# Kernel tuning notes

Hardware: AMD Instinct MI355X
Metric: run time of the kernel (lower is better)

The kernel has to match this reference:

```python
import jax, jax.numpy as jnp
import numpy as np

B, L, D, H = 2, 2048, 1024, 16
DK = D // H  # head_dim = 64


def setup_inputs() -> dict:
    key = jax.random.key(0)
    ks = jax.random.split(key, 12)
    init = lambda k, shape, fan_in: jax.random.uniform(k, shape, jnp.float32, -1.0, 1.0) / np.sqrt(fan_in)
    inp = {
        "query": jax.random.normal(ks[0], (B, L, D), jnp.float32),
        "key": jax.random.normal(ks[1], (B, L, D), jnp.float32),
        "value": jax.random.normal(ks[2], (B, L, D), jnp.float32),
        # causal mask [B, 1, L, L], True = attend
        "mask": jnp.broadcast_to(jnp.tril(jnp.ones((L, L), bool))[None, None], (B, 1, L, L)),
        "wq": init(ks[3], (D, D), D), "bq": jnp.zeros((D,), jnp.float32),
        "wk": init(ks[4], (D, D), D), "bk": jnp.zeros((D,), jnp.float32),
        "wv": init(ks[5], (D, D), D), "bv": jnp.zeros((D,), jnp.float32),
        "wo": init(ks[6], (D, D), D), "bo": jnp.zeros((D,), jnp.float32),
    }
    return inp


def reference(query, key, value, mask, wq, bq, wk, bk, wv, bv, wo, bo):
    b, l, d = query.shape
    split = lambda x: x.reshape(b, l, H, DK).transpose(0, 2, 1, 3)  # B H L dk
    Q = split(query @ wq + bq)
    K = split(key @ wk + bk)
    V = split(value @ wv + bv)
    scores = jnp.einsum("bhqd,bhkd->bhqk", Q, K) / jnp.sqrt(jnp.float32(DK))
    probs = jax.nn.softmax(scores, axis=-1, where=mask)  # masked-out rows contribute 0
    attn = jnp.einsum("bhqk,bhkd->bhqd", probs, V)
    out = attn.transpose(0, 2, 1, 3).reshape(b, l, d)  # B L D
    return out @ wo + bo
```

## Files before the change

kernel.cpp:

```cpp
#include <hip/hip_runtime.h>
#include <hip/hip_bf16.h>

typedef __bf16 bf16x8 __attribute__((ext_vector_type(8)));
typedef __bf16 bf16x4 __attribute__((ext_vector_type(4)));
typedef float floatx4 __attribute__((ext_vector_type(4)));

constexpr int Bn  = 2;
constexpr int Ln  = 2048;
constexpr int Dn  = 1024;
constexpr int Hn  = 16;
constexpr int DKn = 64;
constexpr int Mn  = Bn * Ln;

__device__ __forceinline__ void gload_lds16(const void* g, void* l) {
  __builtin_amdgcn_global_load_lds(
      (const __attribute__((address_space(1))) void*)g,
      (__attribute__((address_space(3))) void*)l, 16, 0, 0);
}

__global__ __launch_bounds__(256) void prep(
    const float* __restrict__ q, const float* __restrict__ k,
    const float* __restrict__ v,
    const float* __restrict__ wq, const float* __restrict__ wk,
    const float* __restrict__ wv, const float* __restrict__ wo,
    __hip_bfloat16* __restrict__ Abf, __hip_bfloat16* __restrict__ wT)
{
  const int z = blockIdx.z;
  __shared__ __bf16 tile[32][33];
  if (z < 3) {
    const float* src = z == 0 ? q : z == 1 ? k : v;
    __hip_bfloat16* d = Abf + (size_t)z * Mn * Dn;
    const int i = blockIdx.x * 256 + threadIdx.x;
    const float4 a = ((const float4*)src)[i * 2];
    const float4 b = ((const float4*)src)[i * 2 + 1];
    bf16x8 o;
    o[0] = (__bf16)a.x; o[1] = (__bf16)a.y; o[2] = (__bf16)a.z; o[3] = (__bf16)a.w;
    o[4] = (__bf16)b.x; o[5] = (__bf16)b.y; o[6] = (__bf16)b.z; o[7] = (__bf16)b.w;
    ((bf16x8*)d)[i] = o;
  } else {
    if (blockIdx.x >= 1024) return;
    const float* src = z == 3 ? wq : z == 4 ? wk : z == 5 ? wv : wo;
    __hip_bfloat16* dst = wT + (size_t)(z - 3) * Dn * Dn;
    const int bx = blockIdx.x & 31, by = blockIdx.x >> 5;
    const int tx = threadIdx.x & 31, ty = threadIdx.x >> 5;
    const int x = bx * 32 + tx, y = by * 32 + ty;
    for (int i = 0; i < 32; i += 8)
      tile[ty + i][tx] = (__bf16)src[(size_t)(y + i) * Dn + x];
    __syncthreads();
    const int x2 = by * 32 + tx, y2 = bx * 32 + ty;
    for (int i = 0; i < 32; i += 8)
      ((__bf16*)dst)[(size_t)(y2 + i) * Dn + x2] = tile[tx][ty + i];
  }
}

__global__ __launch_bounds__(256) void gemm_qkv(
    const __hip_bfloat16* __restrict__ Abf,
    const __hip_bfloat16* __restrict__ wT,
    const float* __restrict__ bq, const float* __restrict__ bk,
    const float* __restrict__ bv,
    __hip_bfloat16* __restrict__ Qp, __hip_bfloat16* __restrict__ Kp,
    __hip_bfloat16* __restrict__ Vt)
{
  constexpr int BK = 32;
  __shared__ __bf16 As[128][BK];
  __shared__ __bf16 Ws[128][BK];
  const int z = blockIdx.z;
  const __hip_bfloat16* A  = Abf + (size_t)z * Mn * Dn;
  const __hip_bfloat16* WT = wT  + (size_t)z * Dn * Dn;
  const float* bias = z == 0 ? bq : z == 1 ? bk : bv;

  const int m0 = blockIdx.x * 128;
  const int n0 = blockIdx.y * 128;
  const int tid  = threadIdx.x;
  const int lane = tid & 63;
  const int wave = tid >> 6;
  const int quad = lane >> 4;
  const int l16  = lane & 15;
  const int wm = (wave >> 1) * 64;
  const int wn = (wave & 1) * 64;
  const int srow = tid >> 2;
  const int scol = (tid & 3) * 8;

  floatx4 acc[4][4];
  for (int i = 0; i < 4; i++)
    for (int j = 0; j < 4; j++)
      acc[i][j] = (floatx4){0.f, 0.f, 0.f, 0.f};

  for (int k0 = 0; k0 < Dn; k0 += BK) {
    for (int half = 0; half < 2; half++) {
      gload_lds16(&A [(size_t)(m0 + srow + half * 64) * Dn + k0 + scol],
                  &As[srow + half * 64][scol]);
      gload_lds16(&WT[(size_t)(n0 + srow + half * 64) * Dn + k0 + scol],
                  &Ws[srow + half * 64][scol]);
    }
    __syncthreads();
    bf16x8 af[4], wf[4];
    for (int i = 0; i < 4; i++) af[i] = *(const bf16x8*)&As[wm + i * 16 + l16][quad * 8];
    for (int j = 0; j < 4; j++) wf[j] = *(const bf16x8*)&Ws[wn + j * 16 + l16][quad * 8];
    if (z == 2) {
      for (int i = 0; i < 4; i++)
        for (int j = 0; j < 4; j++)
          acc[i][j] = __builtin_amdgcn_mfma_f32_16x16x32_bf16(af[i], wf[j], acc[i][j], 0, 0, 0);
    } else {
      for (int i = 0; i < 4; i++)
        for (int j = 0; j < 4; j++)
          acc[i][j] = __builtin_amdgcn_mfma_f32_16x16x32_bf16(wf[j], af[i], acc[i][j], 0, 0, 0);
    }
    __syncthreads();
  }

  if (z == 2) {
    for (int j = 0; j < 4; j++) {
      const int n = n0 + wn + j * 16 + l16;
      const float bvv = bias[n];
      const int h = n >> 6, dk = n & 63;
      for (int i = 0; i < 4; i++) {
        const int m = m0 + wm + i * 16 + quad * 4;
        const int b = m >> 11, li = m & (Ln - 1);
        bf16x4 pk;
        for (int r = 0; r < 4; r++) pk[r] = (__bf16)(acc[i][j][r] + bvv);
        *(bf16x4*)&Vt[(((size_t)(b * Hn + h)) * DKn + dk) * Ln + li] = pk;
      }
    }
  } else {
    __hip_bfloat16* out = z == 0 ? Qp : Kp;
    for (int j = 0; j < 4; j++) {
      const int nq = n0 + wn + j * 16 + quad * 4;
      const float4 b4 = *(const float4*)&bias[nq];
      const int h = nq >> 6, dk = nq & 63;
      for (int i = 0; i < 4; i++) {
        const int m = m0 + wm + i * 16 + l16;
        const int b = m >> 11, li = m & (Ln - 1);
        bf16x4 pk;
        pk[0] = (__bf16)(acc[i][j][0] + b4.x);
        pk[1] = (__bf16)(acc[i][j][1] + b4.y);
        pk[2] = (__bf16)(acc[i][j][2] + b4.z);
        pk[3] = (__bf16)(acc[i][j][3] + b4.w);
        *(bf16x4*)&out[(((size_t)(b * Hn + h)) * Ln + li) * DKn + dk] = pk;
      }
    }
  }
}

__global__ __launch_bounds__(256) void gemm_out(
    const __hip_bfloat16* __restrict__ A,
    const __hip_bfloat16* __restrict__ WT,
    const float* __restrict__ bias,
    float* __restrict__ out)
{
  constexpr int BK = 32;
  __shared__ __bf16 As[128][BK];
  __shared__ __bf16 Ws[64][BK];
  const int m0 = blockIdx.x * 128;
  const int n0 = blockIdx.y * 64;
  const int tid  = threadIdx.x;
  const int lane = tid & 63;
  const int wave = tid >> 6;
  const int quad = lane >> 4;
  const int l16  = lane & 15;
  const int wm = (wave >> 1) * 64;
  const int wn = (wave & 1) * 32;
  const int srow = tid >> 2;
  const int scol = (tid & 3) * 8;

  floatx4 acc[4][2];
  for (int i = 0; i < 4; i++)
    for (int j = 0; j < 2; j++)
      acc[i][j] = (floatx4){0.f, 0.f, 0.f, 0.f};

  for (int k0 = 0; k0 < Dn; k0 += BK) {
    for (int half = 0; half < 2; half++)
      gload_lds16(&A [(size_t)(m0 + srow + half * 64) * Dn + k0 + scol],
                  &As[srow + half * 64][scol]);
    gload_lds16(&WT[(size_t)(n0 + srow) * Dn + k0 + scol], &Ws[srow][scol]);
    __syncthreads();
    bf16x8 af[4], wf[2];
    for (int i = 0; i < 4; i++) af[i] = *(const bf16x8*)&As[wm + i * 16 + l16][quad * 8];
    for (int j = 0; j < 2; j++) wf[j] = *(const bf16x8*)&Ws[wn + j * 16 + l16][quad * 8];
    for (int i = 0; i < 4; i++)
      for (int j = 0; j < 2; j++)
        acc[i][j] = __builtin_amdgcn_mfma_f32_16x16x32_bf16(af[i], wf[j], acc[i][j], 0, 0, 0);
    __syncthreads();
  }

  for (int j = 0; j < 2; j++) {
    const int n = n0 + wn + j * 16 + l16;
    const float bvv = bias[n];
    for (int i = 0; i < 4; i++)
      for (int r = 0; r < 4; r++) {
        const int m = m0 + wm + i * 16 + quad * 4 + r;
        out[(size_t)m * Dn + n] = acc[i][j][r] + bvv;
      }
  }
}

__global__ __launch_bounds__(128) void attn_flash(
    const __hip_bfloat16* __restrict__ Qp,
    const __hip_bfloat16* __restrict__ Kp,
    const __hip_bfloat16* __restrict__ Vt,
    __hip_bfloat16* __restrict__ attn)
{
  const int bh   = blockIdx.x;
  const int qt   = gridDim.y - 1 - blockIdx.y;
  const int tid  = threadIdx.x;
  const int wave = tid >> 6;
  const int lane = tid & 63;
  const int quad = lane >> 4;
  const int l16  = lane & 15;
  const int qw   = qt * 64 + wave * 32;

  const __hip_bfloat16* Qh = Qp + (size_t)bh * Ln * DKn;
  const __hip_bfloat16* Kh = Kp + (size_t)bh * Ln * DKn;
  const __hip_bfloat16* Vh = Vt + (size_t)bh * DKn * Ln;

  __shared__ __align__(16) __bf16 Ks[64][64];
  __shared__ __align__(16) __bf16 Vs[64][64];
  __shared__ __align__(16) __bf16 Plds[2][2][16][72];

  const int srow8 = lane >> 3;
  const int gch   = (lane & 7) ^ srow8;
  const int xs    = l16 & 7;
  const int b = bh >> 4, h = bh & 15;

  auto stage = [&](int kt) {
    for (int s = 0; s < 4; s++) {
      const int u = wave * 4 + s;
      gload_lds16(Kh + (size_t)(kt + u * 8 + srow8) * DKn + gch * 8,
                  &Ks[u * 8][0] + (size_t)lane * 8);
      gload_lds16(Vh + (size_t)(u * 8 + srow8) * Ln + kt + gch * 8,
                  &Vs[u * 8][0] + (size_t)lane * 8);
    }
  };

  bf16x8 qf[2][2];
  for (int m = 0; m < 2; m++)
    for (int dd = 0; dd < 2; dd++)
      qf[m][dd] = *(const bf16x8*)&Qh[(size_t)(qw + m * 16 + l16) * DKn + dd * 32 + quad * 8];

  floatx4 o[2][4];
  for (int m = 0; m < 2; m++)
    for (int t = 0; t < 4; t++) o[m][t] = (floatx4){0.f, 0.f, 0.f, 0.f};
  float lp[2] = {0.f, 0.f};

  stage(0);
  const int iters = qt + 1;
  for (int it = 0; it < iters; it++) {
    const int kt = it * 64;
    __syncthreads();

    bf16x8 kf[4][2], vf[4][2];
    for (int sub = 0; sub < 4; sub++)
      for (int dd = 0; dd < 2; dd++)
        kf[sub][dd] = *(const bf16x8*)&Ks[sub * 16 + l16][((dd * 4 + quad) ^ xs) * 8];
    for (int t = 0; t < 4; t++)
      for (int kc = 0; kc < 2; kc++)
        vf[t][kc] = *(const bf16x8*)&Vs[t * 16 + l16][((kc * 4 + quad) ^ xs) * 8];

    __syncthreads();
    if (it + 1 < iters) stage(kt + 64);

    floatx4 s[2][4];
    for (int m = 0; m < 2; m++)
      for (int sub = 0; sub < 4; sub++) s[m][sub] = (floatx4){0.f, 0.f, 0.f, 0.f};
    for (int sub = 0; sub < 4; sub++)
      for (int dd = 0; dd < 2; dd++) {
        s[0][sub] = __builtin_amdgcn_mfma_f32_16x16x32_bf16(kf[sub][dd], qf[0][dd], s[0][sub], 0, 0, 0);
        s[1][sub] = __builtin_amdgcn_mfma_f32_16x16x32_bf16(kf[sub][dd], qf[1][dd], s[1][sub], 0, 0, 0);
      }

    for (int m = 0; m < 2; m++) {
      const bool needmask = (kt + 64 > qw + m * 16);
      const int qg = qw + m * 16 + l16;
      for (int sub = 0; sub < 4; sub++) {
        bf16x4 pk;
        for (int r = 0; r < 4; r++) {
          float sv = s[m][sub][r];
          if (needmask && (kt + sub * 16 + quad * 4 + r > qg)) sv = -1e30f;
          const float e = __builtin_exp2f(__builtin_fmaf(sv, 0.18033688f, -11.5415603f));
          lp[m] += e;
          pk[r] = (__bf16)e;
        }
        *(bf16x4*)&Plds[wave][m][l16][sub * 16 + quad * 4] = pk;
      }
    }
    __asm__ volatile("s_waitcnt lgkmcnt(0)" ::: "memory");

    bf16x8 pf[2][2];
    for (int m = 0; m < 2; m++)
      for (int kc = 0; kc < 2; kc++)
        pf[m][kc] = *(const bf16x8*)&Plds[wave][m][l16][kc * 32 + quad * 8];
    for (int m = 0; m < 2; m++)
      for (int t = 0; t < 4; t++)
        for (int kc = 0; kc < 2; kc++)
          o[m][t] = __builtin_amdgcn_mfma_f32_16x16x32_bf16(vf[t][kc], pf[m][kc], o[m][t], 0, 0, 0);
  }

  for (int m = 0; m < 2; m++) {
    float lf = lp[m];
    lf += __shfl_xor(lf, 16);
    lf += __shfl_xor(lf, 32);
    const float inv = 1.0f / lf;
    const int ql = qw + m * 16 + l16;
    const size_t base = ((size_t)b * Ln + ql) * Dn + h * DKn;
    for (int t = 0; t < 4; t++) {
      bf16x4 pk;
      for (int r = 0; r < 4; r++) pk[r] = (__bf16)(o[m][t][r] * inv);
      *(bf16x4*)&attn[base + t * 16 + quad * 4] = pk;
    }
  }
}

extern "C" void kernel_launch(void* const* d_in, const int* in_sizes, int n_in,
                              void* d_out, int out_size, void* d_ws, size_t ws_size,
                              hipStream_t stream) {
  const float* query = (const float*)d_in[0];
  const float* key_  = (const float*)d_in[1];
  const float* value = (const float*)d_in[2];
  const float* wq = (const float*)d_in[4];
  const float* bq = (const float*)d_in[5];
  const float* wk = (const float*)d_in[6];
  const float* bk = (const float*)d_in[7];
  const float* wv = (const float*)d_in[8];
  const float* bv = (const float*)d_in[9];
  const float* wo = (const float*)d_in[10];
  const float* bo = (const float*)d_in[11];

  const size_t T   = (size_t)Mn * Dn;
  const size_t WSZ = (size_t)Dn * Dn;
  __hip_bfloat16* Abf  = (__hip_bfloat16*)d_ws;
  __hip_bfloat16* Qp   = Abf + 3 * T;
  __hip_bfloat16* Kp   = Qp + T;
  __hip_bfloat16* Vt   = Kp + T;
  __hip_bfloat16* wT   = Vt + T;
  __hip_bfloat16* attn = Abf;

  prep<<<dim3(2048, 1, 7), 256, 0, stream>>>(query, key_, value, wq, wk, wv, wo, Abf, wT);
  gemm_qkv<<<dim3(Mn / 128, Dn / 128, 3), 256, 0, stream>>>(Abf, wT, bq, bk, bv, Qp, Kp, Vt);
  attn_flash<<<dim3(Bn * Hn, Ln / 64), 128, 0, stream>>>(Qp, Kp, Vt, attn);
  gemm_out<<<dim3(Mn / 128, Dn / 64), 256, 0, stream>>>(attn, wT + 3 * WSZ, bo, (float*)d_out);
}
```

Baseline: 263.3 us.

## Fuse activation bf16 conversion into QKV GEMM and use single-wave attention blocks

The separate prep pass that converted the query, key and value activations to bf16 is removed. gemm_qkv now loads the fp32 activations directly, converts them in registers and writes them to a padded LDS tile, while weights still go through async global-to-LDS loads. This removes a full read/write round trip of the activations, at the cost of synchronous fp32 loads inside the GEMM k-loop. Separately, attention blocks now hold one wave covering 32 query rows, doubling the block count to improve causal load balance, but each K/V tile is loaded by more blocks.

```diff
diff --git a/kernel.cpp b/kernel.cpp
--- a/kernel.cpp
+++ b/kernel.cpp
@@ -18,55 +18,41 @@
       (__attribute__((address_space(3))) void*)l, 16, 0, 0);
 }
 
-__global__ __launch_bounds__(256) void prep(
+__global__ __launch_bounds__(256) void prep_w(
+    const float* __restrict__ wq, const float* __restrict__ wk,
+    const float* __restrict__ wv, const float* __restrict__ wo,
+    __hip_bfloat16* __restrict__ wT)
+{
+  const int z = blockIdx.z;
+  const float* src = z == 0 ? wq : z == 1 ? wk : z == 2 ? wv : wo;
+  __hip_bfloat16* dst = wT + (size_t)z * Dn * Dn;
+  __shared__ __bf16 tile[32][33];
+  const int bx = blockIdx.x & 31, by = blockIdx.x >> 5;
+  const int tx = threadIdx.x & 31, ty = threadIdx.x >> 5;
+  const int x = bx * 32 + tx, y = by * 32 + ty;
+  for (int i = 0; i < 32; i += 8)
+    tile[ty + i][tx] = (__bf16)src[(size_t)(y + i) * Dn + x];
+  __syncthreads();
+  const int x2 = by * 32 + tx, y2 = bx * 32 + ty;
+  for (int i = 0; i < 32; i += 8)
+    ((__bf16*)dst)[(size_t)(y2 + i) * Dn + x2] = tile[tx][ty + i];
+}
+
+__global__ __launch_bounds__(256) void gemm_qkv(
     const float* __restrict__ q, const float* __restrict__ k,
     const float* __restrict__ v,
-    const float* __restrict__ wq, const float* __restrict__ wk,
-    const float* __restrict__ wv, const float* __restrict__ wo,
-    __hip_bfloat16* __restrict__ Abf, __hip_bfloat16* __restrict__ wT)
-{
-  const int z = blockIdx.z;
-  __shared__ __bf16 tile[32][33];
-  if (z < 3) {
-    const float* src = z == 0 ? q : z == 1 ? k : v;
-    __hip_bfloat16* d = Abf + (size_t)z * Mn * Dn;
-    const int i = blockIdx.x * 256 + threadIdx.x;
-    const float4 a = ((const float4*)src)[i * 2];
-    const float4 b = ((const float4*)src)[i * 2 + 1];
-    bf16x8 o;
-    o[0] = (__bf16)a.x; o[1] = (__bf16)a.y; o[2] = (__bf16)a.z; o[3] = (__bf16)a.w;
-    o[4] = (__bf16)b.x; o[5] = (__bf16)b.y; o[6] = (__bf16)b.z; o[7] = (__bf16)b.w;
-    ((bf16x8*)d)[i] = o;
-  } else {
-    if (blockIdx.x >= 1024) return;
-    const float* src = z == 3 ? wq : z == 4 ? wk : z == 5 ? wv : wo;
-    __hip_bfloat16* dst = wT + (size_t)(z - 3) * Dn * Dn;
-    const int bx = blockIdx.x & 31, by = blockIdx.x >> 5;
-    const int tx = threadIdx.x & 31, ty = threadIdx.x >> 5;
-    const int x = bx * 32 + tx, y = by * 32 + ty;
-    for (int i = 0; i < 32; i += 8)
-      tile[ty + i][tx] = (__bf16)src[(size_t)(y + i) * Dn + x];
-    __syncthreads();
-    const int x2 = by * 32 + tx, y2 = bx * 32 + ty;
-    for (int i = 0; i < 32; i += 8)
-      ((__bf16*)dst)[(size_t)(y2 + i) * Dn + x2] = tile[tx][ty + i];
-  }
-}
-
-__global__ __launch_bounds__(256) void gemm_qkv(
-    const __hip_bfloat16* __restrict__ Abf,
     const __hip_bfloat16* __restrict__ wT,
     const float* __restrict__ bq, const float* __restrict__ bk,
     const float* __restrict__ bv,
     __hip_bfloat16* __restrict__ Qp, __hip_bfloat16* __restrict__ Kp,
     __hip_bfloat16* __restrict__ Vt)
 {
-  constexpr int BK = 32;
-  __shared__ __bf16 As[128][BK];
+  constexpr int BK = 32, LDA = 40;
+  __shared__ __align__(16) __bf16 As[128][LDA];
   __shared__ __bf16 Ws[128][BK];
   const int z = blockIdx.z;
-  const __hip_bfloat16* A  = Abf + (size_t)z * Mn * Dn;
-  const __hip_bfloat16* WT = wT  + (size_t)z * Dn * Dn;
+  const float* A = z == 0 ? q : z == 1 ? k : v;
+  const __hip_bfloat16* WT = wT + (size_t)z * Dn * Dn;
   const float* bias = z == 0 ? bq : z == 1 ? bk : bv;
 
   const int m0 = blockIdx.x * 128;
@@ -80,6 +66,8 @@
   const int wn = (wave & 1) * 64;
   const int srow = tid >> 2;
   const int scol = (tid & 3) * 8;
+  const int arow = tid >> 1;
+  const int akh  = (tid & 1) * 16;
 
   floatx4 acc[4][4];
   for (int i = 0; i < 4; i++)
@@ -87,12 +75,21 @@
       acc[i][j] = (floatx4){0.f, 0.f, 0.f, 0.f};
 
   for (int k0 = 0; k0 < Dn; k0 += BK) {
-    for (int half = 0; half < 2; half++) {
-      gload_lds16(&A [(size_t)(m0 + srow + half * 64) * Dn + k0 + scol],
-                  &As[srow + half * 64][scol]);
+    for (int half = 0; half < 2; half++)
       gload_lds16(&WT[(size_t)(n0 + srow + half * 64) * Dn + k0 + scol],
                   &Ws[srow + half * 64][scol]);
-    }
+    const float* ap = &A[(size_t)(m0 + arow) * Dn + k0 + akh];
+    const float4 f0 = *(const float4*)(ap + 0);
+    const float4 f1 = *(const float4*)(ap + 4);
+    const float4 f2 = *(const float4*)(ap + 8);
+    const float4 f3 = *(const float4*)(ap + 12);
+    bf16x8 v0, v1;
+    v0[0] = (__bf16)f0.x; v0[1] = (__bf16)f0.y; v0[2] = (__bf16)f0.z; v0[3] = (__bf16)f0.w;
+    v0[4] = (__bf16)f1.x; v0[5] = (__bf16)f1.y; v0[6] = (__bf16)f1.z; v0[7] = (__bf16)f1.w;
+    v1[0] = (__bf16)f2.x; v1[1] = (__bf16)f2.y; v1[2] = (__bf16)f2.z; v1[3] = (__bf16)f2.w;
+    v1[4] = (__bf16)f3.x; v1[5] = (__bf16)f3.y; v1[6] = (__bf16)f3.z; v1[7] = (__bf16)f3.w;
+    *(bf16x8*)&As[arow][akh]     = v0;
+    *(bf16x8*)&As[arow][akh + 8] = v1;
     __syncthreads();
     bf16x8 af[4], wf[4];
     for (int i = 0; i < 4; i++) af[i] = *(const bf16x8*)&As[wm + i * 16 + l16][quad * 8];
@@ -194,7 +191,7 @@
   }
 }
 
-__global__ __launch_bounds__(128) void attn_flash(
+__global__ __launch_bounds__(64) void attn_flash(
     const __hip_bfloat16* __restrict__ Qp,
     const __hip_bfloat16* __restrict__ Kp,
     const __hip_bfloat16* __restrict__ Vt,
@@ -202,12 +199,10 @@
 {
   const int bh   = blockIdx.x;
   const int qt   = gridDim.y - 1 - blockIdx.y;
-  const int tid  = threadIdx.x;
-  const int wave = tid >> 6;
-  const int lane = tid & 63;
+  const int lane = threadIdx.x & 63;
   const int quad = lane >> 4;
   const int l16  = lane & 15;
-  const int qw   = qt * 64 + wave * 32;
+  const int qw   = qt * 32;
 
   const __hip_bfloat16* Qh = Qp + (size_t)bh * Ln * DKn;
   const __hip_bfloat16* Kh = Kp + (size_t)bh * Ln * DKn;
@@ -215,7 +210,7 @@
 
   __shared__ __align__(16) __bf16 Ks[64][64];
   __shared__ __align__(16) __bf16 Vs[64][64];
-  __shared__ __align__(16) __bf16 Plds[2][2][16][72];
+  __shared__ __align__(16) __bf16 Plds[2][16][72];
 
   const int srow8 = lane >> 3;
   const int gch   = (lane & 7) ^ srow8;
@@ -223,8 +218,7 @@
   const int b = bh >> 4, h = bh & 15;
 
   auto stage = [&](int kt) {
-    for (int s = 0; s < 4; s++) {
-      const int u = wave * 4 + s;
+    for (int u = 0; u < 8; u++) {
       gload_lds16(Kh + (size_t)(kt + u * 8 + srow8) * DKn + gch * 8,
                   &Ks[u * 8][0] + (size_t)lane * 8);
       gload_lds16(Vh + (size_t)(u * 8 + srow8) * Ln + kt + gch * 8,
@@ -243,7 +237,7 @@
   float lp[2] = {0.f, 0.f};
 
   stage(0);
-  const int iters = qt + 1;
+  const int iters = (qt >> 1) + 1;
   for (int it = 0; it < iters; it++) {
     const int kt = it * 64;
     __syncthreads();
@@ -280,7 +274,7 @@
           lp[m] += e;
           pk[r] = (__bf16)e;
         }
-        *(bf16x4*)&Plds[wave][m][l16][sub * 16 + quad * 4] = pk;
+        *(bf16x4*)&Plds[m][l16][sub * 16 + quad * 4] = pk;
       }
     }
     __asm__ volatile("s_waitcnt lgkmcnt(0)" ::: "memory");
@@ -288,7 +282,7 @@
     bf16x8 pf[2][2];
     for (int m = 0; m < 2; m++)
       for (int kc = 0; kc < 2; kc++)
-        pf[m][kc] = *(const bf16x8*)&Plds[wave][m][l16][kc * 32 + quad * 8];
+        pf[m][kc] = *(const bf16x8*)&Plds[m][l16][kc * 32 + quad * 8];
     for (int m = 0; m < 2; m++)
       for (int t = 0; t < 4; t++)
         for (int kc = 0; kc < 2; kc++)
@@ -327,15 +321,15 @@
 
   const size_t T   = (size_t)Mn * Dn;
   const size_t WSZ = (size_t)Dn * Dn;
-  __hip_bfloat16* Abf  = (__hip_bfloat16*)d_ws;
-  __hip_bfloat16* Qp   = Abf + 3 * T;
+  __hip_bfloat16* Qp   = (__hip_bfloat16*)d_ws;
   __hip_bfloat16* Kp   = Qp + T;
   __hip_bfloat16* Vt   = Kp + T;
-  __hip_bfloat16* wT   = Vt + T;
-  __hip_bfloat16* attn = Abf;
-
-  prep<<<dim3(2048, 1, 7), 256, 0, stream>>>(query, key_, value, wq, wk, wv, wo, Abf, wT);
-  gemm_qkv<<<dim3(Mn / 128, Dn / 128, 3), 256, 0, stream>>>(Abf, wT, bq, bk, bv, Qp, Kp, Vt);
-  attn_flash<<<dim3(Bn * Hn, Ln / 64), 128, 0, stream>>>(Qp, Kp, Vt, attn);
+  __hip_bfloat16* attn = Vt + T;
+  __hip_bfloat16* wT   = attn + T;
+
+  prep_w<<<dim3(1024, 1, 4), 256, 0, stream>>>(wq, wk, wv, wo, wT);
+  gemm_qkv<<<dim3(Mn / 128, Dn / 128, 3), 256, 0, stream>>>(
+      query, key_, value, wT, bq, bk, bv, Qp, Kp, Vt);
+  attn_flash<<<dim3(Bn * Hn, Ln / 32), 64, 0, stream>>>(Qp, Kp, Vt, attn);
   gemm_out<<<dim3(Mn / 128, Dn / 64), 256, 0, stream>>>(attn, wT + 3 * WSZ, bo, (float*)d_out);
 }
```

After: 299.1 us. 1.14x slower.
